# Performance work log

Hardware: AMD Instinct MI355X
Metric: run time of the kernel (lower is better)

Reference implementation:

```python
import jax, jax.numpy as jnp
import numpy as np

N_NODES = 100000
N_EDGES = 3200000
IN_FEAT = 128
HIDDEN = 32
NUM_LAYERS = 4
K = 35
NODES_PER_GRAPH = 100


def setup_inputs() -> dict:
    key = jax.random.key(0)
    ks = jax.random.split(key, 20)
    inp = {}
    inp['x'] = jax.random.normal(ks[0], (N_NODES, IN_FEAT), dtype=jnp.float32)
    inp['edge_index'] = jax.random.randint(ks[1], (2, N_EDGES), 0, N_NODES, dtype=jnp.int64)
    inp['batch'] = (jnp.arange(N_NODES, dtype=jnp.int64) // NODES_PER_GRAPH)
    # GCNConv weights (PyG: lin weight [in, out], bias [out])
    dims = [IN_FEAT] + [HIDDEN] * NUM_LAYERS
    for i in range(NUM_LAYERS):
        s = 1.0 / np.sqrt(dims[i])
        inp[f'w{i}'] = jax.random.normal(ks[2 + i], (dims[i], HIDDEN), dtype=jnp.float32) * s
        inp[f'b{i}'] = jnp.zeros((HIDDEN,), dtype=jnp.float32)
    # head: Conv1d(128->16,k=1), Conv1d(16->32,k=5), fc1(416->128), fc2(128->1)
    inp['conv1_w'] = jax.random.normal(ks[8], (16, HIDDEN * NUM_LAYERS, 1), dtype=jnp.float32) * (1.0 / np.sqrt(128))
    inp['conv1_b'] = jnp.zeros((16,), dtype=jnp.float32)
    inp['conv2_w'] = jax.random.normal(ks[9], (32, 16, 5), dtype=jnp.float32) * (1.0 / np.sqrt(16 * 5))
    inp['conv2_b'] = jnp.zeros((32,), dtype=jnp.float32)
    lin_in = 32 * (K // 2 - 4)  # 416
    inp['fc1_w'] = jax.random.normal(ks[10], (128, lin_in), dtype=jnp.float32) * (1.0 / np.sqrt(lin_in))
    inp['fc1_b'] = jnp.zeros((128,), dtype=jnp.float32)
    inp['fc2_w'] = jax.random.normal(ks[11], (1, 128), dtype=jnp.float32) * (1.0 / np.sqrt(128))
    inp['fc2_b'] = jnp.zeros((1,), dtype=jnp.float32)
    return inp


def _gcn_conv(x, w, b, src, dst, n):
    # PyG GCNConv: h = x @ W; add self-loops; sym-normalized scatter-add; + bias
    h = x @ w
    deg = jnp.ones((n,), h.dtype).at[dst].add(1.0)  # degree incl. self-loop
    dis = jax.lax.rsqrt(deg)
    coef = dis[src] * dis[dst]  # [E]
    agg = jax.ops.segment_sum(h[src] * coef[:, None], dst, num_segments=n)
    return agg + h / deg[:, None] + b  # self-loop norm = 1/deg


def reference(x, edge_index, batch, w0, b0, w1, b1, w2, b2, w3, b3,
              conv1_w, conv1_b, conv2_w, conv2_b, fc1_w, fc1_b, fc2_w, fc2_b):
    src, dst = edge_index[0], edge_index[1]
    n = x.shape[0]
    xs = []
    h = x
    for w, b in ((w0, b0), (w1, b1), (w2, b2), (w3, b3)):
        h = jnp.tanh(_gcn_conv(h, w, b, src, dst, n))
        xs.append(h)
    feat = jnp.concatenate(xs, axis=1)  # [N, 128]
    # global_sort_pool: graphs are contiguous blocks of NODES_PER_GRAPH nodes
    G = n // NODES_PER_GRAPH
    dense = feat.reshape(G, NODES_PER_GRAPH, -1)
    order = jnp.argsort(-dense[:, :, -1], axis=1)  # descending by last channel
    topk = jnp.take_along_axis(dense, order[:, :, None], axis=1)[:, :K]  # [G,K,128]
    y = topk.transpose(0, 2, 1)  # [G,128,K]
    y = jax.nn.relu(jnp.einsum('oc,gck->gok', conv1_w[:, :, 0], y) + conv1_b[None, :, None])
    L = y.shape[-1] // 2  # MaxPool1d(2), drop trailing element
    y = y[..., :L * 2].reshape(G, 16, L, 2).max(axis=-1)  # [G,16,17]
    y = jax.lax.conv_general_dilated(y, conv2_w, (1,), 'VALID',
                                     dimension_numbers=('NCH', 'OIH', 'NCH'))
    y = jax.nn.relu(y + conv2_b[None, :, None])  # [G,32,13]
    y = y.reshape(G, -1)  # [G,416]
    y = jax.nn.relu(y @ fc1_w.T + fc1_b)  # dropout is identity in eval
    return jax.nn.sigmoid(y @ fc2_w.T + fc2_b)  # [G,1]
```

## Files before the change

### kernel.cpp

```cpp
#include <hip/hip_runtime.h>
#include <hip/hip_fp16.h>
#include <math.h>

#define N_NODES 100000
#define N_EDGES 3200000
#define HIDDEN 32
#define K_TOP 35
#define NPG 100
#define N_GRAPHS 1000

#define BSHIFT 9
#define NLOC 512
#define NBUCK 196
#define CAP 17408
#define NBB 1024
#define BIN_CHUNK 13


__global__ void k_bin(const int* __restrict__ src, const int* __restrict__ dst,
                      int* __restrict__ bcnt, unsigned int* __restrict__ bdata) {
    __shared__ int h[NBUCK];
    __shared__ int lbase[NBUCK];
    __shared__ int lcur[NBUCK];
    int t = threadIdx.x;
    for (int i = t; i < NBUCK; i += 256) { h[i] = 0; lcur[i] = 0; }
    __syncthreads();
    int base = blockIdx.x * (256 * BIN_CHUNK);
    int ss[BIN_CHUNK], ds[BIN_CHUNK];
#pragma unroll
    for (int k = 0; k < BIN_CHUNK; k++) {
        int e = base + k * 256 + t;
        if (e < N_EDGES) {
            ss[k] = src[e];
            ds[k] = dst[e];
            atomicAdd(&h[ds[k] >> BSHIFT], 1);
        } else ds[k] = -1;
    }
    __syncthreads();
    for (int i = t; i < NBUCK; i += 256)
        lbase[i] = h[i] ? atomicAdd(&bcnt[i], h[i]) : 0;
    __syncthreads();
#pragma unroll
    for (int k = 0; k < BIN_CHUNK; k++) {
        int d = ds[k];
        if (d >= 0) {
            int bk = d >> BSHIFT;
            int pos = atomicAdd(&lcur[bk], 1);
            bdata[bk * CAP + lbase[bk] + pos] =
                ((unsigned int)ss[k] << BSHIFT) | (unsigned int)(d & (NLOC - 1));
        }
    }
}

__global__ void k_cnt(const unsigned int* __restrict__ bdata, const int* __restrict__ bcnt,
                      int* __restrict__ cnt, int* __restrict__ row_ptr,
                      float* __restrict__ dis) {
    __shared__ int h[NLOC];
    __shared__ int sd[256];
    int b = blockIdx.x, t = threadIdx.x;
    h[t] = 0; h[t + 256] = 0;
    __syncthreads();
    int r0 = b * CAP, r1 = r0 + bcnt[b];
    for (int i = r0 + t; i < r1; i += 256)
        atomicAdd(&h[bdata[i] & (NLOC - 1)], 1);
    __syncthreads();
    int a0 = h[2 * t], a1 = h[2 * t + 1];
    int ps = a0 + a1;
    sd[t] = ps; __syncthreads();
    for (int off = 1; off < 256; off <<= 1) {
        int x = (t >= off) ? sd[t - off] : 0;
        __syncthreads();
        sd[t] += x;
        __syncthreads();
    }
    int excl = sd[t] - ps;
    int n0 = (b << BSHIFT) + 2 * t;
    if (n0 < N_NODES) {
        cnt[n0] = a0;
        dis[n0] = rsqrtf((float)(a0 + 1));
        row_ptr[n0] = r0 + excl;
    }
    int n1 = n0 + 1;
    if (n1 < N_NODES) {
        cnt[n1] = a1;
        dis[n1] = rsqrtf((float)(a1 + 1));
        row_ptr[n1] = r0 + excl + a0;
    }
}

__global__ void k_csrfill(const unsigned int* __restrict__ bdata, const int* __restrict__ bcnt,
                          const int* __restrict__ row_ptr, int* __restrict__ csr) {
    __shared__ int rp[NLOC];
    __shared__ int cur[NLOC];
    int b = blockIdx.x, t = threadIdx.x;
    int node = (b << BSHIFT) + t;
    rp[t] = (node < N_NODES) ? row_ptr[node] : 0;
    cur[t] = 0;
    __syncthreads();
    int r0 = b * CAP, r1 = r0 + bcnt[b];
    for (int i = r0 + t; i < r1; i += NLOC) {
        unsigned int v = bdata[i];
        int loc = v & (NLOC - 1);
        int pos = atomicAdd(&cur[loc], 1);
        csr[rp[loc] + pos] = (int)(v >> BSHIFT);
    }
}


__global__ void k_mm0(const float* __restrict__ in, const float* __restrict__ w,
                      const float* __restrict__ dis, void* __restrict__ hs) {
    __shared__ float wl[128 * HIDDEN];
    int t = threadIdx.x;
    for (int i = t; i < 128 * HIDDEN; i += 256) wl[i] = w[i];
    __syncthreads();
    int n = blockIdx.x * 256 + t;
    if (n >= N_NODES) return;
    const float* row = in + (size_t)n * 128;
    float acc[HIDDEN];
#pragma unroll
    for (int o = 0; o < HIDDEN; o++) acc[o] = 0.f;
    for (int c4 = 0; c4 < 32; c4++) {
        float4 v = *(const float4*)(row + c4 * 4);
        float xv[4] = {v.x, v.y, v.z, v.w};
#pragma unroll
        for (int k = 0; k < 4; k++) {
            const float* wr = &wl[(c4 * 4 + k) * HIDDEN];
#pragma unroll
            for (int o = 0; o < HIDDEN; o++) acc[o] += xv[k] * wr[o];
        }
    }
    float d = dis[n];
    float4* hr = (float4*)((char*)hs + (size_t)n * 64);
#pragma unroll
    for (int qq = 0; qq < 4; qq++) {
        __half2 p[4];
#pragma unroll
        for (int k = 0; k < 4; k++)
            p[k] = __floats2half2_rn(acc[8 * qq + 2 * k] * d, acc[8 * qq + 2 * k + 1] * d);
        hr[qq] = *(float4*)p;
    }
}

__global__ void k_agg(const float4* __restrict__ hs4, const float* __restrict__ dis,
                      const int* __restrict__ row_ptr, const int* __restrict__ cnt,
                      const int* __restrict__ csr_src, const float* __restrict__ bias,
                      float* __restrict__ feat, int col_off,
                      const float* __restrict__ wnext, void* __restrict__ hsn) {
    __shared__ float wl[32 * 33];
    __shared__ float tv[8][36];
    int tt = threadIdx.x;
    if (wnext) {
        for (int i = tt; i < 1024; i += 256)
            wl[(i >> 5) * 33 + (i & 31)] = wnext[i];
    }
    __syncthreads();
    int n = (blockIdx.x * 256 + tt) >> 5;
    int c = tt & 31;
    int q = c >> 2, r = c & 3;
    int start = row_ptr[n];
    int m = cnt[n];
    float a0=0,a1=0,a2=0,a3=0,a4=0,a5=0,a6=0,a7=0;
    float b0=0,b1=0,b2=0,b3=0,b4=0,b5=0,b6=0,b7=0;
    int j = q;
    for (; j + 8 < m; j += 16) {
        int s0 = csr_src[start + j];
        int s1 = csr_src[start + j + 8];
        float4 v0 = hs4[(size_t)s0 * 4 + r];
        float4 v1 = hs4[(size_t)s1 * 4 + r];
        const __half2* h0 = (const __half2*)&v0;
        const __half2* h1 = (const __half2*)&v1;
        float2 f;
        f = __half22float2(h0[0]); a0 += f.x; a1 += f.y;
        f = __half22float2(h0[1]); a2 += f.x; a3 += f.y;
        f = __half22float2(h0[2]); a4 += f.x; a5 += f.y;
        f = __half22float2(h0[3]); a6 += f.x; a7 += f.y;
        f = __half22float2(h1[0]); b0 += f.x; b1 += f.y;
        f = __half22float2(h1[1]); b2 += f.x; b3 += f.y;
        f = __half22float2(h1[2]); b4 += f.x; b5 += f.y;
        f = __half22float2(h1[3]); b6 += f.x; b7 += f.y;
    }
    if (j < m) {
        int s0 = csr_src[start + j];
        float4 v0 = hs4[(size_t)s0 * 4 + r];
        const __half2* h0 = (const __half2*)&v0;
        float2 f;
        f = __half22float2(h0[0]); a0 += f.x; a1 += f.y;
        f = __half22float2(h0[1]); a2 += f.x; a3 += f.y;
        f = __half22float2(h0[2]); a4 += f.x; a5 += f.y;
        f = __half22float2(h0[3]); a6 += f.x; a7 += f.y;
    }
    float s[8];
    s[0]=a0+b0; s[1]=a1+b1; s[2]=a2+b2; s[3]=a3+b3;
    s[4]=a4+b4; s[5]=a5+b5; s[6]=a6+b6; s[7]=a7+b7;
#pragma unroll
    for (int k = 0; k < 8; k++) {
        float v = s[k];
        v += __shfl_xor(v, 4);
        v += __shfl_xor(v, 8);
        v += __shfl_xor(v, 16);
        s[k] = v;
    }
    float d = dis[n];
    int slot = tt >> 5;
    if (q == 0) {
        float4 sv = hs4[(size_t)n * 4 + r];
        const __half2* sh = (const __half2*)&sv;
        const float* bb = bias + 8 * r;
        float ov[8];
#pragma unroll
        for (int k = 0; k < 4; k++) {
            float2 f = __half22float2(sh[k]);
            ov[2 * k]     = tanhf(d * (s[2 * k]     + f.x) + bb[2 * k]);
            ov[2 * k + 1] = tanhf(d * (s[2 * k + 1] + f.y) + bb[2 * k + 1]);
        }
        float* fr = feat + (size_t)n * 128 + col_off + 8 * r;
        *(float4*)fr       = make_float4(ov[0], ov[1], ov[2], ov[3]);
        *(float4*)(fr + 4) = make_float4(ov[4], ov[5], ov[6], ov[7]);
        if (wnext) {
            *(float4*)&tv[slot][8 * r]     = make_float4(ov[0], ov[1], ov[2], ov[3]);
            *(float4*)&tv[slot][8 * r + 4] = make_float4(ov[4], ov[5], ov[6], ov[7]);
        }
    }
    if (wnext) {
        __builtin_amdgcn_wave_barrier();
        float o = 0.f;
#pragma unroll 8
        for (int k = 0; k < 32; k++)
            o += tv[slot][k] * wl[k * 33 + c];
        o *= d;
        float oh = __shfl_xor(o, 1);
        if ((c & 1) == 0) {
            __half2 p = __floats2half2_rn(o, oh);
            *((__half2*)((char*)hsn + (size_t)n * 64 + 2 * c)) = p;
        }
    }
}


__global__ void __launch_bounds__(256, 4)
k_head(const float* __restrict__ feat,
       const float* __restrict__ c1w, const float* __restrict__ c1b,
       const float* __restrict__ c2w, const float* __restrict__ c2b,
       const float* __restrict__ f1w, const float* __restrict__ f1b,
       const float* __restrict__ f2w, const float* __restrict__ f2b,
       float* __restrict__ out) {
    __shared__ float vals[NPG];
    __shared__ int sel[K_TOP];
    __shared__ float tk[K_TOP * 132];
    __shared__ float wl1[16 * 129];
    __shared__ float y1[16][36];
    __shared__ float y2[16][17];
    __shared__ float y3[416];
    __shared__ float y4[128];
    __shared__ float r2[128];
    int g = blockIdx.x, t = threadIdx.x;
    const float* fg = feat + (size_t)g * NPG * 128;

    for (int i = t; i < 2048; i += 256)
        wl1[(i >> 7) * 129 + (i & 127)] = c1w[i];
    if (t < NPG) vals[t] = fg[t * 128 + 127];
    __syncthreads();
    if (t < NPG) {
        float v = vals[t];
        int r = 0;
        for (int j = 0; j < NPG; j++) {
            float u = vals[j];
            r += (u > v) || (u == v && j < t);
        }
        if (r < K_TOP) sel[r] = t;
    }
    __syncthreads();
    for (int i = t; i < K_TOP * 32; i += 256) {
        int k = i >> 5, c4 = i & 31;
        *(float4*)&tk[k * 132 + 4 * c4] = *(const float4*)&fg[sel[k] * 128 + 4 * c4];
    }
    __syncthreads();
    for (int i = t; i < 16 * K_TOP; i += 256) {
        int o = i & 15, k = i >> 4;
        float s = c1b[o];
        const float* wr = &wl1[o * 129];
        const float* xr = &tk[k * 132];
#pragma unroll 8
        for (int c = 0; c < 128; c++) s += wr[c] * xr[c];
        y1[o][k] = fmaxf(s, 0.f);
    }
    __syncthreads();
    for (int i = t; i < 16 * 17; i += 256) {
        int o = i & 15, l = i >> 4;
        y2[o][l] = fmaxf(y1[o][2 * l], y1[o][2 * l + 1]);
    }
    __syncthreads();
    for (int idx = t; idx < 32 * 13; idx += 256) {
        int o2 = idx / 13, ttp = idx - o2 * 13;
        float s = c2b[o2];
        const float* wr = c2w + o2 * 80;
#pragma unroll
        for (int i = 0; i < 16; i++)
#pragma unroll
            for (int j = 0; j < 5; j++) s += wr[i * 5 + j] * y2[i][ttp + j];
        y3[idx] = fmaxf(s, 0.f);
    }
    __syncthreads();
    {
        int o = t >> 1, h = t & 1;
        const float4* wr4 = (const float4*)(f1w + o * 416) + h * 52;
        const float* yb = y3 + h * 208;
        float s = 0.f;
#pragma unroll 4
        for (int i = 0; i < 52; i++) {
            float4 w4 = wr4[i];
            s += w4.x * yb[4 * i] + w4.y * yb[4 * i + 1] +
                 w4.z * yb[4 * i + 2] + w4.w * yb[4 * i + 3];
        }
        s += __shfl_xor(s, 1);
        if (h == 0) y4[o] = fmaxf(s + f1b[o], 0.f);
    }
    __syncthreads();
    if (t < 128) r2[t] = f2w[t] * y4[t];
    __syncthreads();
    for (int off = 64; off > 0; off >>= 1) {
        if (t < off) r2[t] += r2[t + off];
        __syncthreads();
    }
    if (t == 0) out[g] = 1.0f / (1.0f + expf(-(r2[0] + f2b[0])));
}


static inline size_t alignup(size_t x) { return (x + 255) & ~(size_t)255; }

extern "C" void kernel_launch(void* const* d_in, const int* in_sizes, int n_in,
                              void* d_out, int out_size, void* d_ws, size_t ws_size,
                              hipStream_t stream) {
    const float* x    = (const float*)d_in[0];
    const int*   ei   = (const int*)d_in[1];
    const int*   srcp = ei;
    const int*   dstp = ei + N_EDGES;
    const float* w0 = (const float*)d_in[3];
    const float* b0 = (const float*)d_in[4];
    const float* w1 = (const float*)d_in[5];
    const float* b1 = (const float*)d_in[6];
    const float* w2 = (const float*)d_in[7];
    const float* b2 = (const float*)d_in[8];
    const float* w3 = (const float*)d_in[9];
    const float* b3 = (const float*)d_in[10];
    const float* c1w = (const float*)d_in[11];
    const float* c1b = (const float*)d_in[12];
    const float* c2w = (const float*)d_in[13];
    const float* c2b = (const float*)d_in[14];
    const float* f1w = (const float*)d_in[15];
    const float* f1b = (const float*)d_in[16];
    const float* f2w = (const float*)d_in[17];
    const float* f2b = (const float*)d_in[18];
    float* out = (float*)d_out;

    char* p = (char*)d_ws;
    int* cnt     = (int*)p; p += alignup(sizeof(int) * N_NODES);
    int* row_ptr = (int*)p; p += alignup(sizeof(int) * N_NODES);
    float* dis   = (float*)p; p += alignup(sizeof(float) * N_NODES);
    int* bcnt    = (int*)p; p += alignup(sizeof(int) * NBUCK);
    int* csr     = (int*)p; p += alignup(sizeof(int) * (size_t)NBUCK * CAP);
    char* U = p;
    unsigned int* bdata = (unsigned int*)U;
    void* hsA = (void*)U;
    void* hsB = (void*)(U + alignup((size_t)N_NODES * 64));
    size_t usz = alignup(sizeof(unsigned int) * (size_t)NBUCK * CAP);
    float* feat = (float*)(U + usz);

    const int NB_N = (N_NODES + 255) / 256;
    const int NB_A = (N_NODES * 32) / 256;

    hipMemsetAsync(bcnt, 0, sizeof(int) * NBUCK, stream);
    k_bin<<<NBB, 256, 0, stream>>>(srcp, dstp, bcnt, bdata);
    k_cnt<<<NBUCK, 256, 0, stream>>>(bdata, bcnt, cnt, row_ptr, dis);
    k_csrfill<<<NBUCK, NLOC, 0, stream>>>(bdata, bcnt, row_ptr, csr);

    k_mm0<<<NB_N, 256, 0, stream>>>(x, w0, dis, hsA);
    k_agg<<<NB_A, 256, 0, stream>>>((const float4*)hsA, dis, row_ptr, cnt, csr, b0,
                                    feat, 0, w1, hsB);
    k_agg<<<NB_A, 256, 0, stream>>>((const float4*)hsB, dis, row_ptr, cnt, csr, b1,
                                    feat, 32, w2, hsA);
    k_agg<<<NB_A, 256, 0, stream>>>((const float4*)hsA, dis, row_ptr, cnt, csr, b2,
                                    feat, 64, w3, hsB);
    k_agg<<<NB_A, 256, 0, stream>>>((const float4*)hsB, dis, row_ptr, cnt, csr, b3,
                                    feat, 96, (const float*)nullptr, (void*)nullptr);

    k_head<<<N_GRAPHS, 256, 0, stream>>>(feat, c1w, c1b, c2w, c2b,
                                         f1w, f1b, f2w, f2b, out);
}
```

Baseline: 481.1 us.

## Split fp16 hidden features into two half-planes and aggregate in two passes

The fp16 hidden-state buffer is split into two separate planes, each holding 16 channels (32 bytes per node). The aggregation kernel now gathers one plane per pass, caching the neighbor indices in LDS during the first pass so the second pass can reuse them. Each gather touches a smaller working set, which is meant to improve cache hit rates for random neighbor reads. The count and CSR-fill kernels are also fused into one, and feature writes and index loads use nontemporal hints; in exchange the aggregation does two passes and more shuffle reductions.

```diff
diff --git a/kernel.cpp b/kernel.cpp
--- a/kernel.cpp
+++ b/kernel.cpp
@@ -15,6 +15,10 @@
 #define CAP 17408
 #define NBB 1024
 #define BIN_CHUNK 13
+#define CACHE_E 128
+#define HS_HALF ((size_t)N_NODES * 32)
+
+typedef float vfloat4 __attribute__((ext_vector_type(4)));
 
 
 __global__ void k_bin(const int* __restrict__ src, const int* __restrict__ dst,
@@ -52,63 +56,49 @@
     }
 }
 
-__global__ void k_cnt(const unsigned int* __restrict__ bdata, const int* __restrict__ bcnt,
-                      int* __restrict__ cnt, int* __restrict__ row_ptr,
-                      float* __restrict__ dis) {
+__global__ void k_build(const unsigned int* __restrict__ bdata, const int* __restrict__ bcnt,
+                        int* __restrict__ cnt, int* __restrict__ row_ptr,
+                        float* __restrict__ dis, int* __restrict__ csr) {
     __shared__ int h[NLOC];
-    __shared__ int sd[256];
+    __shared__ int sd[NLOC];
+    __shared__ int rp[NLOC];
+    __shared__ int cur[NLOC];
     int b = blockIdx.x, t = threadIdx.x;
-    h[t] = 0; h[t + 256] = 0;
+    h[t] = 0;
     __syncthreads();
     int r0 = b * CAP, r1 = r0 + bcnt[b];
-    for (int i = r0 + t; i < r1; i += 256)
+    for (int i = r0 + t; i < r1; i += NLOC)
         atomicAdd(&h[bdata[i] & (NLOC - 1)], 1);
     __syncthreads();
-    int a0 = h[2 * t], a1 = h[2 * t + 1];
-    int ps = a0 + a1;
-    sd[t] = ps; __syncthreads();
-    for (int off = 1; off < 256; off <<= 1) {
+    int v = h[t];
+    sd[t] = v; __syncthreads();
+    for (int off = 1; off < NLOC; off <<= 1) {
         int x = (t >= off) ? sd[t - off] : 0;
         __syncthreads();
         sd[t] += x;
         __syncthreads();
     }
-    int excl = sd[t] - ps;
-    int n0 = (b << BSHIFT) + 2 * t;
-    if (n0 < N_NODES) {
-        cnt[n0] = a0;
-        dis[n0] = rsqrtf((float)(a0 + 1));
-        row_ptr[n0] = r0 + excl;
-    }
-    int n1 = n0 + 1;
-    if (n1 < N_NODES) {
-        cnt[n1] = a1;
-        dis[n1] = rsqrtf((float)(a1 + 1));
-        row_ptr[n1] = r0 + excl + a0;
-    }
-}
-
-__global__ void k_csrfill(const unsigned int* __restrict__ bdata, const int* __restrict__ bcnt,
-                          const int* __restrict__ row_ptr, int* __restrict__ csr) {
-    __shared__ int rp[NLOC];
-    __shared__ int cur[NLOC];
-    int b = blockIdx.x, t = threadIdx.x;
+    int excl = sd[t] - v;
     int node = (b << BSHIFT) + t;
-    rp[t] = (node < N_NODES) ? row_ptr[node] : 0;
+    rp[t] = r0 + excl;
     cur[t] = 0;
-    __syncthreads();
-    int r0 = b * CAP, r1 = r0 + bcnt[b];
+    if (node < N_NODES) {
+        cnt[node] = v;
+        dis[node] = rsqrtf((float)(v + 1));
+        row_ptr[node] = r0 + excl;
+    }
+    __syncthreads();
     for (int i = r0 + t; i < r1; i += NLOC) {
-        unsigned int v = bdata[i];
-        int loc = v & (NLOC - 1);
+        unsigned int u = bdata[i];
+        int loc = u & (NLOC - 1);
         int pos = atomicAdd(&cur[loc], 1);
-        csr[rp[loc] + pos] = (int)(v >> BSHIFT);
+        csr[rp[loc] + pos] = (int)(u >> BSHIFT);
     }
 }
 
 
 __global__ void k_mm0(const float* __restrict__ in, const float* __restrict__ w,
-                      const float* __restrict__ dis, void* __restrict__ hs) {
+                      const float* __restrict__ dis, char* __restrict__ hs) {
     __shared__ float wl[128 * HIDDEN];
     int t = threadIdx.x;
     for (int i = t; i < 128 * HIDDEN; i += 256) wl[i] = w[i];
@@ -130,24 +120,27 @@
         }
     }
     float d = dis[n];
-    float4* hr = (float4*)((char*)hs + (size_t)n * 64);
-#pragma unroll
-    for (int qq = 0; qq < 4; qq++) {
-        __half2 p[4];
-#pragma unroll
-        for (int k = 0; k < 4; k++)
-            p[k] = __floats2half2_rn(acc[8 * qq + 2 * k] * d, acc[8 * qq + 2 * k + 1] * d);
-        hr[qq] = *(float4*)p;
-    }
-}
-
-__global__ void k_agg(const float4* __restrict__ hs4, const float* __restrict__ dis,
+    __half2 pl[8], ph[8];
+#pragma unroll
+    for (int k = 0; k < 8; k++) {
+        pl[k] = __floats2half2_rn(acc[2 * k] * d, acc[2 * k + 1] * d);
+        ph[k] = __floats2half2_rn(acc[16 + 2 * k] * d, acc[17 + 2 * k] * d);
+    }
+    float4* lo = (float4*)(hs + (size_t)n * 32);
+    float4* hi = (float4*)(hs + HS_HALF + (size_t)n * 32);
+    lo[0] = ((float4*)pl)[0]; lo[1] = ((float4*)pl)[1];
+    hi[0] = ((float4*)ph)[0]; hi[1] = ((float4*)ph)[1];
+}
+
+__global__ void k_agg(const float4* __restrict__ glo, const float4* __restrict__ ghi,
+                      const float* __restrict__ dis,
                       const int* __restrict__ row_ptr, const int* __restrict__ cnt,
                       const int* __restrict__ csr_src, const float* __restrict__ bias,
                       float* __restrict__ feat, int col_off,
-                      const float* __restrict__ wnext, void* __restrict__ hsn) {
+                      const float* __restrict__ wnext, char* __restrict__ hsn) {
     __shared__ float wl[32 * 33];
     __shared__ float tv[8][36];
+    __shared__ int ec[8][CACHE_E];
     int tt = threadIdx.x;
     if (wnext) {
         for (int i = tt; i < 1024; i += 256)
@@ -156,69 +149,122 @@
     __syncthreads();
     int n = (blockIdx.x * 256 + tt) >> 5;
     int c = tt & 31;
-    int q = c >> 2, r = c & 3;
+    int q = c >> 1, r = c & 1;
+    int slot = tt >> 5;
     int start = row_ptr[n];
     int m = cnt[n];
-    float a0=0,a1=0,a2=0,a3=0,a4=0,a5=0,a6=0,a7=0;
-    float b0=0,b1=0,b2=0,b3=0,b4=0,b5=0,b6=0,b7=0;
-    int j = q;
-    for (; j + 8 < m; j += 16) {
-        int s0 = csr_src[start + j];
-        int s1 = csr_src[start + j + 8];
-        float4 v0 = hs4[(size_t)s0 * 4 + r];
-        float4 v1 = hs4[(size_t)s1 * 4 + r];
-        const __half2* h0 = (const __half2*)&v0;
-        const __half2* h1 = (const __half2*)&v1;
-        float2 f;
-        f = __half22float2(h0[0]); a0 += f.x; a1 += f.y;
-        f = __half22float2(h0[1]); a2 += f.x; a3 += f.y;
-        f = __half22float2(h0[2]); a4 += f.x; a5 += f.y;
-        f = __half22float2(h0[3]); a6 += f.x; a7 += f.y;
-        f = __half22float2(h1[0]); b0 += f.x; b1 += f.y;
-        f = __half22float2(h1[1]); b2 += f.x; b3 += f.y;
-        f = __half22float2(h1[2]); b4 += f.x; b5 += f.y;
-        f = __half22float2(h1[3]); b6 += f.x; b7 += f.y;
-    }
-    if (j < m) {
-        int s0 = csr_src[start + j];
-        float4 v0 = hs4[(size_t)s0 * 4 + r];
-        const __half2* h0 = (const __half2*)&v0;
-        float2 f;
-        f = __half22float2(h0[0]); a0 += f.x; a1 += f.y;
-        f = __half22float2(h0[1]); a2 += f.x; a3 += f.y;
-        f = __half22float2(h0[2]); a4 += f.x; a5 += f.y;
-        f = __half22float2(h0[3]); a6 += f.x; a7 += f.y;
-    }
-    float s[8];
-    s[0]=a0+b0; s[1]=a1+b1; s[2]=a2+b2; s[3]=a3+b3;
-    s[4]=a4+b4; s[5]=a5+b5; s[6]=a6+b6; s[7]=a7+b7;
+    float sA[8], sB[8];
+
+    {
+        float a0=0,a1=0,a2=0,a3=0,a4=0,a5=0,a6=0,a7=0;
+        float b0=0,b1=0,b2=0,b3=0,b4=0,b5=0,b6=0,b7=0;
+        int j = q;
+        for (; j + 16 < m; j += 32) {
+            int s0 = __builtin_nontemporal_load(&csr_src[start + j]);
+            int s1 = __builtin_nontemporal_load(&csr_src[start + j + 16]);
+            if (r == 0) {
+                if (j < CACHE_E) ec[slot][j] = s0;
+                if (j + 16 < CACHE_E) ec[slot][j + 16] = s1;
+            }
+            float4 v0 = glo[(size_t)s0 * 2 + r];
+            float4 v1 = glo[(size_t)s1 * 2 + r];
+            const __half2* h0 = (const __half2*)&v0;
+            const __half2* h1 = (const __half2*)&v1;
+            float2 f;
+            f = __half22float2(h0[0]); a0 += f.x; a1 += f.y;
+            f = __half22float2(h0[1]); a2 += f.x; a3 += f.y;
+            f = __half22float2(h0[2]); a4 += f.x; a5 += f.y;
+            f = __half22float2(h0[3]); a6 += f.x; a7 += f.y;
+            f = __half22float2(h1[0]); b0 += f.x; b1 += f.y;
+            f = __half22float2(h1[1]); b2 += f.x; b3 += f.y;
+            f = __half22float2(h1[2]); b4 += f.x; b5 += f.y;
+            f = __half22float2(h1[3]); b6 += f.x; b7 += f.y;
+        }
+        if (j < m) {
+            int s0 = __builtin_nontemporal_load(&csr_src[start + j]);
+            if (r == 0 && j < CACHE_E) ec[slot][j] = s0;
+            float4 v0 = glo[(size_t)s0 * 2 + r];
+            const __half2* h0 = (const __half2*)&v0;
+            float2 f;
+            f = __half22float2(h0[0]); a0 += f.x; a1 += f.y;
+            f = __half22float2(h0[1]); a2 += f.x; a3 += f.y;
+            f = __half22float2(h0[2]); a4 += f.x; a5 += f.y;
+            f = __half22float2(h0[3]); a6 += f.x; a7 += f.y;
+        }
+        sA[0]=a0+b0; sA[1]=a1+b1; sA[2]=a2+b2; sA[3]=a3+b3;
+        sA[4]=a4+b4; sA[5]=a5+b5; sA[6]=a6+b6; sA[7]=a7+b7;
+    }
+    __builtin_amdgcn_wave_barrier();
+    {
+        float a0=0,a1=0,a2=0,a3=0,a4=0,a5=0,a6=0,a7=0;
+        float b0=0,b1=0,b2=0,b3=0,b4=0,b5=0,b6=0,b7=0;
+        int j = q;
+        for (; j + 16 < m; j += 32) {
+            int s0, s1;
+            if (j < CACHE_E) s0 = ec[slot][j]; else s0 = csr_src[start + j];
+            if (j + 16 < CACHE_E) s1 = ec[slot][j + 16]; else s1 = csr_src[start + j + 16];
+            float4 v0 = ghi[(size_t)s0 * 2 + r];
+            float4 v1 = ghi[(size_t)s1 * 2 + r];
+            const __half2* h0 = (const __half2*)&v0;
+            const __half2* h1 = (const __half2*)&v1;
+            float2 f;
+            f = __half22float2(h0[0]); a0 += f.x; a1 += f.y;
+            f = __half22float2(h0[1]); a2 += f.x; a3 += f.y;
+            f = __half22float2(h0[2]); a4 += f.x; a5 += f.y;
+            f = __half22float2(h0[3]); a6 += f.x; a7 += f.y;
+            f = __half22float2(h1[0]); b0 += f.x; b1 += f.y;
+            f = __half22float2(h1[1]); b2 += f.x; b3 += f.y;
+            f = __half22float2(h1[2]); b4 += f.x; b5 += f.y;
+            f = __half22float2(h1[3]); b6 += f.x; b7 += f.y;
+        }
+        if (j < m) {
+            int s0;
+            if (j < CACHE_E) s0 = ec[slot][j]; else s0 = csr_src[start + j];
+            float4 v0 = ghi[(size_t)s0 * 2 + r];
+            const __half2* h0 = (const __half2*)&v0;
+            float2 f;
+            f = __half22float2(h0[0]); a0 += f.x; a1 += f.y;
+            f = __half22float2(h0[1]); a2 += f.x; a3 += f.y;
+            f = __half22float2(h0[2]); a4 += f.x; a5 += f.y;
+            f = __half22float2(h0[3]); a6 += f.x; a7 += f.y;
+        }
+        sB[0]=a0+b0; sB[1]=a1+b1; sB[2]=a2+b2; sB[3]=a3+b3;
+        sB[4]=a4+b4; sB[5]=a5+b5; sB[6]=a6+b6; sB[7]=a7+b7;
+    }
 #pragma unroll
     for (int k = 0; k < 8; k++) {
-        float v = s[k];
-        v += __shfl_xor(v, 4);
-        v += __shfl_xor(v, 8);
-        v += __shfl_xor(v, 16);
-        s[k] = v;
+        float v = sA[k];
+        v += __shfl_xor(v, 2); v += __shfl_xor(v, 4);
+        v += __shfl_xor(v, 8); v += __shfl_xor(v, 16);
+        sA[k] = v;
+        float u = sB[k];
+        u += __shfl_xor(u, 2); u += __shfl_xor(u, 4);
+        u += __shfl_xor(u, 8); u += __shfl_xor(u, 16);
+        sB[k] = u;
     }
     float d = dis[n];
-    int slot = tt >> 5;
-    if (q == 0) {
-        float4 sv = hs4[(size_t)n * 4 + r];
+    if (c < 4) {
+        const float4* st = (c < 2) ? glo : ghi;
+        float4 sv = st[(size_t)n * 2 + (c & 1)];
         const __half2* sh = (const __half2*)&sv;
-        const float* bb = bias + 8 * r;
+        float se[8];
+#pragma unroll
+        for (int k = 0; k < 8; k++) se[k] = (c < 2) ? sA[k] : sB[k];
         float ov[8];
 #pragma unroll
         for (int k = 0; k < 4; k++) {
             float2 f = __half22float2(sh[k]);
-            ov[2 * k]     = tanhf(d * (s[2 * k]     + f.x) + bb[2 * k]);
-            ov[2 * k + 1] = tanhf(d * (s[2 * k + 1] + f.y) + bb[2 * k + 1]);
-        }
-        float* fr = feat + (size_t)n * 128 + col_off + 8 * r;
-        *(float4*)fr       = make_float4(ov[0], ov[1], ov[2], ov[3]);
-        *(float4*)(fr + 4) = make_float4(ov[4], ov[5], ov[6], ov[7]);
+            ov[2 * k]     = tanhf(d * (se[2 * k]     + f.x) + bias[8 * c + 2 * k]);
+            ov[2 * k + 1] = tanhf(d * (se[2 * k + 1] + f.y) + bias[8 * c + 2 * k + 1]);
+        }
+        float* fr = feat + (size_t)n * 128 + col_off + 8 * c;
+        vfloat4 o0 = {ov[0], ov[1], ov[2], ov[3]};
+        vfloat4 o1 = {ov[4], ov[5], ov[6], ov[7]};
+        __builtin_nontemporal_store(o0, (vfloat4*)fr);
+        __builtin_nontemporal_store(o1, (vfloat4*)(fr + 4));
         if (wnext) {
-            *(float4*)&tv[slot][8 * r]     = make_float4(ov[0], ov[1], ov[2], ov[3]);
-            *(float4*)&tv[slot][8 * r + 4] = make_float4(ov[4], ov[5], ov[6], ov[7]);
+            *(float4*)&tv[slot][8 * c]     = make_float4(ov[0], ov[1], ov[2], ov[3]);
+            *(float4*)&tv[slot][8 * c + 4] = make_float4(ov[4], ov[5], ov[6], ov[7]);
         }
     }
     if (wnext) {
@@ -230,8 +276,10 @@
         o *= d;
         float oh = __shfl_xor(o, 1);
         if ((c & 1) == 0) {
-            __half2 p = __floats2half2_rn(o, oh);
-            *((__half2*)((char*)hsn + (size_t)n * 64 + 2 * c)) = p;
+            __half2 pck = __floats2half2_rn(o, oh);
+            char* bp = hsn + ((c < 16) ? ((size_t)n * 32 + (size_t)c * 2)
+                                       : (HS_HALF + (size_t)n * 32 + (size_t)(c - 16) * 2));
+            *(__half2*)bp = pck;
         }
     }
 }
@@ -361,8 +409,8 @@
     int* csr     = (int*)p; p += alignup(sizeof(int) * (size_t)NBUCK * CAP);
     char* U = p;
     unsigned int* bdata = (unsigned int*)U;
-    void* hsA = (void*)U;
-    void* hsB = (void*)(U + alignup((size_t)N_NODES * 64));
+    char* hsA = U;
+    char* hsB = U + alignup(2 * HS_HALF);
     size_t usz = alignup(sizeof(unsigned int) * (size_t)NBUCK * CAP);
     float* feat = (float*)(U + usz);
 
@@ -371,18 +419,18 @@
 
     hipMemsetAsync(bcnt, 0, sizeof(int) * NBUCK, stream);
     k_bin<<<NBB, 256, 0, stream>>>(srcp, dstp, bcnt, bdata);
-    k_cnt<<<NBUCK, 256, 0, stream>>>(bdata, bcnt, cnt, row_ptr, dis);
-    k_csrfill<<<NBUCK, NLOC, 0, stream>>>(bdata, bcnt, row_ptr, csr);
+    k_build<<<NBUCK, NLOC, 0, stream>>>(bdata, bcnt, cnt, row_ptr, dis, csr);
 
     k_mm0<<<NB_N, 256, 0, stream>>>(x, w0, dis, hsA);
-    k_agg<<<NB_A, 256, 0, stream>>>((const float4*)hsA, dis, row_ptr, cnt, csr, b0,
-                                    feat, 0, w1, hsB);
-    k_agg<<<NB_A, 256, 0, stream>>>((const float4*)hsB, dis, row_ptr, cnt, csr, b1,
-                                    feat, 32, w2, hsA);
-    k_agg<<<NB_A, 256, 0, stream>>>((const float4*)hsA, dis, row_ptr, cnt, csr, b2,
-                                    feat, 64, w3, hsB);
-    k_agg<<<NB_A, 256, 0, stream>>>((const float4*)hsB, dis, row_ptr, cnt, csr, b3,
-                                    feat, 96, (const float*)nullptr, (void*)nullptr);
+    k_agg<<<NB_A, 256, 0, stream>>>((const float4*)hsA, (const float4*)(hsA + HS_HALF),
+                                    dis, row_ptr, cnt, csr, b0, feat, 0, w1, hsB);
+    k_agg<<<NB_A, 256, 0, stream>>>((const float4*)hsB, (const float4*)(hsB + HS_HALF),
+                                    dis, row_ptr, cnt, csr, b1, feat, 32, w2, hsA);
+    k_agg<<<NB_A, 256, 0, stream>>>((const float4*)hsA, (const float4*)(hsA + HS_HALF),
+                                    dis, row_ptr, cnt, csr, b2, feat, 64, w3, hsB);
+    k_agg<<<NB_A, 256, 0, stream>>>((const float4*)hsB, (const float4*)(hsB + HS_HALF),
+                                    dis, row_ptr, cnt, csr, b3, feat, 96,
+                                    (const float*)nullptr, (char*)nullptr);
 
     k_head<<<N_GRAPHS, 256, 0, stream>>>(feat, c1w, c1b, c2w, c2b,
                                          f1w, f1b, f2w, f2b, out);
```

Result: slower. 550.0 us (+14.3%).

## Fuse CSR count and fill kernels; coalesce neighbor index loads via shuffles

Applied to the files above, without the earlier changes.

Merges the degree-count/scan kernel and the CSR fill kernel into one block-per-bucket kernel with 512 threads, so the bucket is scanned and filled without a second launch or a row_ptr round trip. The aggregation kernel now loads 32 neighbor indices per wave in one coalesced read and broadcasts them with shuffles, issuing four gathers per iteration instead of two strided index loads. Feature writes use nontemporal stores. Each gather iteration is predicated, so low-degree nodes pay for some masked lanes.

```diff
diff --git a/kernel.cpp b/kernel.cpp
--- a/kernel.cpp
+++ b/kernel.cpp
@@ -15,6 +15,8 @@
 #define CAP 17408
 #define NBB 1024
 #define BIN_CHUNK 13
+
+typedef float vfloat4 __attribute__((ext_vector_type(4)));
 
 
 __global__ void k_bin(const int* __restrict__ src, const int* __restrict__ dst,
@@ -52,63 +54,49 @@
     }
 }
 
-__global__ void k_cnt(const unsigned int* __restrict__ bdata, const int* __restrict__ bcnt,
-                      int* __restrict__ cnt, int* __restrict__ row_ptr,
-                      float* __restrict__ dis) {
+__global__ void k_build(const unsigned int* __restrict__ bdata, const int* __restrict__ bcnt,
+                        int* __restrict__ cnt, int* __restrict__ row_ptr,
+                        float* __restrict__ dis, int* __restrict__ csr) {
     __shared__ int h[NLOC];
-    __shared__ int sd[256];
+    __shared__ int sd[NLOC];
+    __shared__ int rp[NLOC];
+    __shared__ int cur[NLOC];
     int b = blockIdx.x, t = threadIdx.x;
-    h[t] = 0; h[t + 256] = 0;
+    h[t] = 0;
     __syncthreads();
     int r0 = b * CAP, r1 = r0 + bcnt[b];
-    for (int i = r0 + t; i < r1; i += 256)
+    for (int i = r0 + t; i < r1; i += NLOC)
         atomicAdd(&h[bdata[i] & (NLOC - 1)], 1);
     __syncthreads();
-    int a0 = h[2 * t], a1 = h[2 * t + 1];
-    int ps = a0 + a1;
-    sd[t] = ps; __syncthreads();
-    for (int off = 1; off < 256; off <<= 1) {
+    int v = h[t];
+    sd[t] = v; __syncthreads();
+    for (int off = 1; off < NLOC; off <<= 1) {
         int x = (t >= off) ? sd[t - off] : 0;
         __syncthreads();
         sd[t] += x;
         __syncthreads();
     }
-    int excl = sd[t] - ps;
-    int n0 = (b << BSHIFT) + 2 * t;
-    if (n0 < N_NODES) {
-        cnt[n0] = a0;
-        dis[n0] = rsqrtf((float)(a0 + 1));
-        row_ptr[n0] = r0 + excl;
-    }
-    int n1 = n0 + 1;
-    if (n1 < N_NODES) {
-        cnt[n1] = a1;
-        dis[n1] = rsqrtf((float)(a1 + 1));
-        row_ptr[n1] = r0 + excl + a0;
-    }
-}
-
-__global__ void k_csrfill(const unsigned int* __restrict__ bdata, const int* __restrict__ bcnt,
-                          const int* __restrict__ row_ptr, int* __restrict__ csr) {
-    __shared__ int rp[NLOC];
-    __shared__ int cur[NLOC];
-    int b = blockIdx.x, t = threadIdx.x;
+    int excl = sd[t] - v;
     int node = (b << BSHIFT) + t;
-    rp[t] = (node < N_NODES) ? row_ptr[node] : 0;
+    rp[t] = r0 + excl;
     cur[t] = 0;
-    __syncthreads();
-    int r0 = b * CAP, r1 = r0 + bcnt[b];
+    if (node < N_NODES) {
+        cnt[node] = v;
+        dis[node] = rsqrtf((float)(v + 1));
+        row_ptr[node] = r0 + excl;
+    }
+    __syncthreads();
     for (int i = r0 + t; i < r1; i += NLOC) {
-        unsigned int v = bdata[i];
-        int loc = v & (NLOC - 1);
+        unsigned int u = bdata[i];
+        int loc = u & (NLOC - 1);
         int pos = atomicAdd(&cur[loc], 1);
-        csr[rp[loc] + pos] = (int)(v >> BSHIFT);
+        csr[rp[loc] + pos] = (int)(u >> BSHIFT);
     }
 }
 
 
 __global__ void k_mm0(const float* __restrict__ in, const float* __restrict__ w,
-                      const float* __restrict__ dis, void* __restrict__ hs) {
+                      const float* __restrict__ dis, char* __restrict__ hs) {
     __shared__ float wl[128 * HIDDEN];
     int t = threadIdx.x;
     for (int i = t; i < 128 * HIDDEN; i += 256) wl[i] = w[i];
@@ -130,7 +118,7 @@
         }
     }
     float d = dis[n];
-    float4* hr = (float4*)((char*)hs + (size_t)n * 64);
+    float4* hr = (float4*)(hs + (size_t)n * 64);
 #pragma unroll
     for (int qq = 0; qq < 4; qq++) {
         __half2 p[4];
@@ -145,7 +133,7 @@
                       const int* __restrict__ row_ptr, const int* __restrict__ cnt,
                       const int* __restrict__ csr_src, const float* __restrict__ bias,
                       float* __restrict__ feat, int col_off,
-                      const float* __restrict__ wnext, void* __restrict__ hsn) {
+                      const float* __restrict__ wnext, char* __restrict__ hsn) {
     __shared__ float wl[32 * 33];
     __shared__ float tv[8][36];
     int tt = threadIdx.x;
@@ -156,69 +144,87 @@
     __syncthreads();
     int n = (blockIdx.x * 256 + tt) >> 5;
     int c = tt & 31;
-    int q = c >> 2, r = c & 3;
+    int r = c & 3;
+    int ph = c >> 2;
+    int slot = tt >> 5;
     int start = row_ptr[n];
     int m = cnt[n];
-    float a0=0,a1=0,a2=0,a3=0,a4=0,a5=0,a6=0,a7=0;
-    float b0=0,b1=0,b2=0,b3=0,b4=0,b5=0,b6=0,b7=0;
-    int j = q;
-    for (; j + 8 < m; j += 16) {
-        int s0 = csr_src[start + j];
-        int s1 = csr_src[start + j + 8];
-        float4 v0 = hs4[(size_t)s0 * 4 + r];
-        float4 v1 = hs4[(size_t)s1 * 4 + r];
-        const __half2* h0 = (const __half2*)&v0;
-        const __half2* h1 = (const __half2*)&v1;
+    float d = dis[n];
+    float aA[8] = {0, 0, 0, 0, 0, 0, 0, 0};
+    float aB[8] = {0, 0, 0, 0, 0, 0, 0, 0};
+
+    for (int base = 0; base < m; base += 32) {
+        int e = base + c;
+        int idx = (e < m) ? csr_src[start + e] : 0;
+        int id0 = __shfl(idx, ph, 32);
+        int id1 = __shfl(idx, 8 + ph, 32);
+        int id2 = __shfl(idx, 16 + ph, 32);
+        int id3 = __shfl(idx, 24 + ph, 32);
+        bool v0 = base + ph < m;
+        bool v1 = base + 8 + ph < m;
+        bool v2 = base + 16 + ph < m;
+        bool v3 = base + 24 + ph < m;
+        float4 g0 = hs4[(size_t)(v0 ? id0 : n) * 4 + r];
+        float4 g1 = hs4[(size_t)(v1 ? id1 : n) * 4 + r];
+        float4 g2 = hs4[(size_t)(v2 ? id2 : n) * 4 + r];
+        float4 g3 = hs4[(size_t)(v3 ? id3 : n) * 4 + r];
+        const __half2* h0 = (const __half2*)&g0;
+        const __half2* h1 = (const __half2*)&g1;
+        const __half2* h2 = (const __half2*)&g2;
+        const __half2* h3 = (const __half2*)&g3;
         float2 f;
-        f = __half22float2(h0[0]); a0 += f.x; a1 += f.y;
-        f = __half22float2(h0[1]); a2 += f.x; a3 += f.y;
-        f = __half22float2(h0[2]); a4 += f.x; a5 += f.y;
-        f = __half22float2(h0[3]); a6 += f.x; a7 += f.y;
-        f = __half22float2(h1[0]); b0 += f.x; b1 += f.y;
-        f = __half22float2(h1[1]); b2 += f.x; b3 += f.y;
-        f = __half22float2(h1[2]); b4 += f.x; b5 += f.y;
-        f = __half22float2(h1[3]); b6 += f.x; b7 += f.y;
-    }
-    if (j < m) {
-        int s0 = csr_src[start + j];
-        float4 v0 = hs4[(size_t)s0 * 4 + r];
-        const __half2* h0 = (const __half2*)&v0;
-        float2 f;
-        f = __half22float2(h0[0]); a0 += f.x; a1 += f.y;
-        f = __half22float2(h0[1]); a2 += f.x; a3 += f.y;
-        f = __half22float2(h0[2]); a4 += f.x; a5 += f.y;
-        f = __half22float2(h0[3]); a6 += f.x; a7 += f.y;
+        if (v0) {
+            f = __half22float2(h0[0]); aA[0] += f.x; aA[1] += f.y;
+            f = __half22float2(h0[1]); aA[2] += f.x; aA[3] += f.y;
+            f = __half22float2(h0[2]); aA[4] += f.x; aA[5] += f.y;
+            f = __half22float2(h0[3]); aA[6] += f.x; aA[7] += f.y;
+        }
+        if (v1) {
+            f = __half22float2(h1[0]); aB[0] += f.x; aB[1] += f.y;
+            f = __half22float2(h1[1]); aB[2] += f.x; aB[3] += f.y;
+            f = __half22float2(h1[2]); aB[4] += f.x; aB[5] += f.y;
+            f = __half22float2(h1[3]); aB[6] += f.x; aB[7] += f.y;
+        }
+        if (v2) {
+            f = __half22float2(h2[0]); aA[0] += f.x; aA[1] += f.y;
+            f = __half22float2(h2[1]); aA[2] += f.x; aA[3] += f.y;
+            f = __half22float2(h2[2]); aA[4] += f.x; aA[5] += f.y;
+            f = __half22float2(h2[3]); aA[6] += f.x; aA[7] += f.y;
+        }
+        if (v3) {
+            f = __half22float2(h3[0]); aB[0] += f.x; aB[1] += f.y;
+            f = __half22float2(h3[1]); aB[2] += f.x; aB[3] += f.y;
+            f = __half22float2(h3[2]); aB[4] += f.x; aB[5] += f.y;
+            f = __half22float2(h3[3]); aB[6] += f.x; aB[7] += f.y;
+        }
     }
     float s[8];
-    s[0]=a0+b0; s[1]=a1+b1; s[2]=a2+b2; s[3]=a3+b3;
-    s[4]=a4+b4; s[5]=a5+b5; s[6]=a6+b6; s[7]=a7+b7;
 #pragma unroll
     for (int k = 0; k < 8; k++) {
-        float v = s[k];
+        float v = aA[k] + aB[k];
         v += __shfl_xor(v, 4);
         v += __shfl_xor(v, 8);
         v += __shfl_xor(v, 16);
         s[k] = v;
     }
-    float d = dis[n];
-    int slot = tt >> 5;
-    if (q == 0) {
+    if (c < 4) {
         float4 sv = hs4[(size_t)n * 4 + r];
         const __half2* sh = (const __half2*)&sv;
-        const float* bb = bias + 8 * r;
         float ov[8];
 #pragma unroll
         for (int k = 0; k < 4; k++) {
             float2 f = __half22float2(sh[k]);
-            ov[2 * k]     = tanhf(d * (s[2 * k]     + f.x) + bb[2 * k]);
-            ov[2 * k + 1] = tanhf(d * (s[2 * k + 1] + f.y) + bb[2 * k + 1]);
-        }
-        float* fr = feat + (size_t)n * 128 + col_off + 8 * r;
-        *(float4*)fr       = make_float4(ov[0], ov[1], ov[2], ov[3]);
-        *(float4*)(fr + 4) = make_float4(ov[4], ov[5], ov[6], ov[7]);
+            ov[2 * k]     = tanhf(d * (s[2 * k]     + f.x) + bias[8 * c + 2 * k]);
+            ov[2 * k + 1] = tanhf(d * (s[2 * k + 1] + f.y) + bias[8 * c + 2 * k + 1]);
+        }
+        float* fr = feat + (size_t)n * 128 + col_off + 8 * c;
+        vfloat4 o0 = {ov[0], ov[1], ov[2], ov[3]};
+        vfloat4 o1 = {ov[4], ov[5], ov[6], ov[7]};
+        __builtin_nontemporal_store(o0, (vfloat4*)fr);
+        __builtin_nontemporal_store(o1, (vfloat4*)(fr + 4));
         if (wnext) {
-            *(float4*)&tv[slot][8 * r]     = make_float4(ov[0], ov[1], ov[2], ov[3]);
-            *(float4*)&tv[slot][8 * r + 4] = make_float4(ov[4], ov[5], ov[6], ov[7]);
+            *(float4*)&tv[slot][8 * c]     = make_float4(ov[0], ov[1], ov[2], ov[3]);
+            *(float4*)&tv[slot][8 * c + 4] = make_float4(ov[4], ov[5], ov[6], ov[7]);
         }
     }
     if (wnext) {
@@ -230,8 +236,8 @@
         o *= d;
         float oh = __shfl_xor(o, 1);
         if ((c & 1) == 0) {
-            __half2 p = __floats2half2_rn(o, oh);
-            *((__half2*)((char*)hsn + (size_t)n * 64 + 2 * c)) = p;
+            __half2 pck = __floats2half2_rn(o, oh);
+            *(__half2*)(hsn + (size_t)n * 64 + (size_t)c * 2) = pck;
         }
     }
 }
@@ -361,8 +367,8 @@
     int* csr     = (int*)p; p += alignup(sizeof(int) * (size_t)NBUCK * CAP);
     char* U = p;
     unsigned int* bdata = (unsigned int*)U;
-    void* hsA = (void*)U;
-    void* hsB = (void*)(U + alignup((size_t)N_NODES * 64));
+    char* hsA = U;
+    char* hsB = U + alignup((size_t)N_NODES * 64);
     size_t usz = alignup(sizeof(unsigned int) * (size_t)NBUCK * CAP);
     float* feat = (float*)(U + usz);
 
@@ -371,8 +377,7 @@
 
     hipMemsetAsync(bcnt, 0, sizeof(int) * NBUCK, stream);
     k_bin<<<NBB, 256, 0, stream>>>(srcp, dstp, bcnt, bdata);
-    k_cnt<<<NBUCK, 256, 0, stream>>>(bdata, bcnt, cnt, row_ptr, dis);
-    k_csrfill<<<NBUCK, NLOC, 0, stream>>>(bdata, bcnt, row_ptr, csr);
+    k_build<<<NBUCK, NLOC, 0, stream>>>(bdata, bcnt, cnt, row_ptr, dis, csr);
 
     k_mm0<<<NB_N, 256, 0, stream>>>(x, w0, dis, hsA);
     k_agg<<<NB_A, 256, 0, stream>>>((const float4*)hsA, dis, row_ptr, cnt, csr, b0,
@@ -382,7 +387,7 @@
     k_agg<<<NB_A, 256, 0, stream>>>((const float4*)hsA, dis, row_ptr, cnt, csr, b2,
                                     feat, 64, w3, hsB);
     k_agg<<<NB_A, 256, 0, stream>>>((const float4*)hsB, dis, row_ptr, cnt, csr, b3,
-                                    feat, 96, (const float*)nullptr, (void*)nullptr);
+                                    feat, 96, (const float*)nullptr, (char*)nullptr);
 
     k_head<<<N_GRAPHS, 256, 0, stream>>>(feat, c1w, c1b, c2w, c2b,
                                          f1w, f1b, f2w, f2b, out);
```

Result: faster. 460.8 us (-4.2%).
